# Performance work log

Hardware: AMD Instinct MI355X
Metric: run time of the kernel (lower is better)

## Reference

```python
import jax, jax.numpy as jnp
import numpy as np
from jax import lax

V, H, B, S, NSLOT, T, G, NSW = 20000, 400, 16, 256, 30, 10, 3, 40


def setup_inputs() -> dict:
    key = jax.random.key(0)
    ks = jax.random.split(key, 24)
    p = lambda k, shape: jax.random.normal(k, shape, dtype=jnp.float32) * 0.1
    return {
        'story': jax.random.randint(ks[0], (B, S), 0, V),
        'enc_lens': jax.random.randint(ks[1], (B,), S // 2, S + 1),
        'target_batches': jax.random.randint(ks[2], (B, NSLOT, T), 0, V),
        'domain_idx': jax.random.randint(ks[3], (NSLOT,), 0, NSW),
        'slot_idx': jax.random.randint(ks[4], (NSLOT,), 0, NSW),
        'emb': p(ks[5], (V, H)),
        'enc_Wih_f': p(ks[6], (3 * H, H)), 'enc_Whh_f': p(ks[7], (3 * H, H)),
        'enc_bih_f': p(ks[8], (3 * H,)), 'enc_bhh_f': p(ks[9], (3 * H,)),
        'enc_Wih_b': p(ks[10], (3 * H, H)), 'enc_Whh_b': p(ks[11], (3 * H, H)),
        'enc_bih_b': p(ks[12], (3 * H,)), 'enc_bhh_b': p(ks[13], (3 * H,)),
        'dec_Wih': p(ks[14], (3 * H, H)), 'dec_Whh': p(ks[15], (3 * H, H)),
        'dec_bih': p(ks[16], (3 * H,)), 'dec_bhh': p(ks[17], (3 * H,)),
        'Wr': p(ks[18], (1, 3 * H)), 'br': p(ks[19], (1,)),
        'Wg': p(ks[20], (G, H)), 'bg': p(ks[21], (G,)),
        'slot_table': p(ks[22], (NSW, H)),
    }


def _gru_scan(x, m, h0, Wih, Whh, bih, bhh):
    # x: [S,B,H], m: [S,B] validity mask (packed-sequence semantics)
    def step(h, xm):
        xt, mt = xm
        gi = xt @ Wih.T + bih
        gh = h @ Whh.T + bhh
        ir, iz, inn = jnp.split(gi, 3, -1)
        hr, hz, hn = jnp.split(gh, 3, -1)
        r = jax.nn.sigmoid(ir + hr)
        z = jax.nn.sigmoid(iz + hz)
        n = jnp.tanh(inn + r * hn)
        hnew = (1.0 - z) * n + z * h
        h = jnp.where(mt[:, None], hnew, h)
        y = jnp.where(mt[:, None], hnew, 0.0)
        return h, y
    hT, ys = lax.scan(step, h0, (x, m))
    return ys, hT


def reference(story, enc_lens, target_batches, domain_idx, slot_idx, emb,
              enc_Wih_f, enc_Whh_f, enc_bih_f, enc_bhh_f,
              enc_Wih_b, enc_Whh_b, enc_bih_b, enc_bhh_b,
              dec_Wih, dec_Whh, dec_bih, dec_bhh,
              Wr, br, Wg, bg, slot_table):
    Bc, Sc = story.shape
    nslot = domain_idx.shape[0]
    Tc = target_batches.shape[2]
    NB = nslot * Bc

    # ----- EncoderRNN: bidirectional GRU over story (seq-major) -----
    x = emb[story.T]                                   # [S,B,H]
    mask = jnp.arange(Sc)[:, None] < enc_lens[None, :]  # [S,B]
    h0 = jnp.zeros((Bc, H), jnp.float32)
    ys_f, h_f = _gru_scan(x, mask, h0, enc_Wih_f, enc_Whh_f, enc_bih_f, enc_bhh_f)
    ys_b, h_b = _gru_scan(x[::-1], mask[::-1], h0, enc_Wih_b, enc_Whh_b, enc_bih_b, enc_bhh_b)
    ys_b = ys_b[::-1]
    encoded_outputs = (ys_f + ys_b).transpose(1, 0, 2)  # [B,S,H]
    enc_hidden = h_f + h_b                              # [B,H]

    # ----- Generator (parallel decode, teacher forcing) -----
    combined = slot_table[domain_idx] + slot_table[slot_idx]           # [nslot,H]
    slot_emb_arr = jnp.repeat(combined[:, None, :], Bc, axis=1).reshape(NB, H)
    hidden0 = jnp.tile(enc_hidden, (nslot, 1))                         # [NB,H]
    enc_out = jnp.tile(encoded_outputs, (nslot, 1, 1))                 # [NB,S,H]
    lens_rep = jnp.tile(enc_lens, nslot)
    story_rep = jnp.tile(story, (nslot, 1))                            # [NB,S]
    attn_mask = jnp.arange(Sc)[None, :] < lens_rep[:, None]            # [NB,S]
    rows = jnp.arange(NB)[:, None]

    # teacher-forced decoder inputs: step0 = slot emb, then gold tokens
    tgt_flat = target_batches.transpose(1, 0, 2).reshape(NB, Tc)       # [NB,T]
    dec_in = jnp.concatenate([slot_emb_arr[None], emb[tgt_flat[:, :Tc - 1].T]], axis=0)  # [T,NB,H]

    def dec_step(h, x_in):
        gi = x_in @ dec_Wih.T + dec_bih
        gh = h @ dec_Whh.T + dec_bhh
        ir, iz, inn = jnp.split(gi, 3, -1)
        hr, hz, hn = jnp.split(gh, 3, -1)
        r = jax.nn.sigmoid(ir + hr)
        z = jax.nn.sigmoid(iz + hz)
        n = jnp.tanh(inn + r * hn)
        h = (1.0 - z) * n + z * h                      # dec_state == new hidden
        scores = jnp.einsum('nh,nsh->ns', h, enc_out)
        scores = jnp.where(attn_mask, scores, -jnp.inf)
        prob = jax.nn.softmax(scores, axis=1)          # [NB,S]
        context = jnp.einsum('ns,nsh->nh', prob, enc_out)
        p_vocab = jax.nn.softmax(h @ emb.T, axis=1)    # [NB,V]
        p_gen_vec = jnp.concatenate([h, context, x_in], axis=-1)
        sw = jax.nn.sigmoid(p_gen_vec @ Wr.T + br)     # [NB,1]
        p_ctx = jnp.zeros_like(p_vocab).at[rows, story_rep].add(prob)
        final_p = (1.0 - sw) * p_ctx + sw * p_vocab
        return h, (final_p, context)

    _, (finals, contexts) = lax.scan(dec_step, hidden0, dec_in)
    all_point_outputs = finals.reshape(Tc, nslot, Bc, V).transpose(1, 2, 0, 3)  # [nslot,B,T,V]
    all_gate_outputs = (contexts[0] @ Wg.T + bg).reshape(nslot, Bc, G)
    return all_point_outputs, all_gate_outputs
```

## Files before the change

kernel.cpp:

```cpp
#include <hip/hip_runtime.h>
#include <hip/hip_bf16.h>

typedef unsigned short u16;
typedef __attribute__((ext_vector_type(8))) short bf16x8;
typedef __attribute__((ext_vector_type(4))) float f32x4;
typedef __attribute__((ext_vector_type(4))) unsigned u32x4;

static constexpr int V = 20000, H = 400, B = 16, S = 256, NSLOT = 30, T = 10, G = 3;
static constexpr int H3 = 3 * H;
static constexpr int NB = NSLOT * B;
static constexpr int MM = T * NB;
static constexpr int ENBLK = 20;
static constexpr int ESL   = 20;
static constexpr int EROWS = 64;
static constexpr int EKP   = 416;
static constexpr int ENC_BLOCKS = 2 * ENBLK;
static constexpr int DGI_TM = (MM + 63) / 64;
static constexpr int DGI_TN = (H3 + 63) / 64;
static constexpr int DGI_TILES = DGI_TM * DGI_TN;
static constexpr int HP2 = 424;
static constexpr int SCP = 260;
static constexpr int PP  = 264;
static constexpr int CXP = 404;
static constexpr int FUSED_LDS = 32*HP2*2 + 32*SCP*4 + 32*PP*2 + 32*CXP*4;
static constexpr int NE = V * H;
static constexpr int NW = H3 * H;
static constexpr int NP = 2 * ENBLK * EROWS * EKP;

__device__ __forceinline__ float bf2f(u16 v) {
    union { unsigned u; float f; } x; x.u = ((unsigned)v) << 16; return x.f;
}
__device__ __forceinline__ u16 f2bf(float f) {
    union { float f; unsigned u; } x; x.f = f;
    unsigned r = x.u + 0x7fffu + ((x.u >> 16) & 1u);
    return (u16)(r >> 16);
}
__device__ __forceinline__ float sigm(float v) { return 1.f / (1.f + __expf(-v)); }

__global__ __launch_bounds__(256) void gemm_bt(
    const u16* __restrict__ A, const u16* __restrict__ Bt,
    const float* __restrict__ bias, float* __restrict__ C,
    int M, int N, int K, int lda, int ldb, long long ldc)
{
    __shared__ u16 As[64][40];
    __shared__ u16 Bs[64][40];
    const int m0 = blockIdx.x * 64, n0 = blockIdx.y * 64;
    const int tid = threadIdx.x, wave = tid >> 6, lane = tid & 63;
    const int wm = (wave >> 1) * 32, wn = (wave & 1) * 32;
    const int srow = tid >> 2, scol = (tid & 3) * 8;
    const int fr = lane & 15, kq = lane >> 4;
    f32x4 acc[2][2];
#pragma unroll
    for (int i = 0; i < 2; ++i)
#pragma unroll
        for (int j = 0; j < 2; ++j) acc[i][j] = (f32x4){0.f, 0.f, 0.f, 0.f};

    for (int k0 = 0; k0 < K; k0 += 32) {
        {
            int gr = m0 + srow, gc = k0 + scol;
            bf16x8 v;
            if (gr < M && gc + 8 <= K) {
                v = *(const bf16x8*)(A + (long long)gr * lda + gc);
            } else {
                short tmp[8];
#pragma unroll
                for (int j = 0; j < 8; ++j)
                    tmp[j] = (gr < M && gc + j < K) ? (short)A[(long long)gr * lda + gc + j] : (short)0;
                v = *(bf16x8*)tmp;
            }
            *(bf16x8*)&As[srow][scol] = v;
        }
        {
            int gr = n0 + srow, gc = k0 + scol;
            bf16x8 v;
            if (gr < N && gc + 8 <= K) {
                v = *(const bf16x8*)(Bt + (long long)gr * ldb + gc);
            } else {
                short tmp[8];
#pragma unroll
                for (int j = 0; j < 8; ++j)
                    tmp[j] = (gr < N && gc + j < K) ? (short)Bt[(long long)gr * ldb + gc + j] : (short)0;
                v = *(bf16x8*)tmp;
            }
            *(bf16x8*)&Bs[srow][scol] = v;
        }
        __syncthreads();
        bf16x8 af[2], bfr[2];
#pragma unroll
        for (int i = 0; i < 2; ++i) af[i]  = *(const bf16x8*)&As[wm + i * 16 + fr][kq * 8];
#pragma unroll
        for (int j = 0; j < 2; ++j) bfr[j] = *(const bf16x8*)&Bs[wn + j * 16 + fr][kq * 8];
#pragma unroll
        for (int i = 0; i < 2; ++i)
#pragma unroll
            for (int j = 0; j < 2; ++j)
                acc[i][j] = __builtin_amdgcn_mfma_f32_16x16x32_bf16(af[i], bfr[j], acc[i][j], 0, 0, 0);
        __syncthreads();
    }

#pragma unroll
    for (int i = 0; i < 2; ++i)
#pragma unroll
        for (int j = 0; j < 2; ++j) {
            int col = n0 + wn + j * 16 + fr;
            float bv = (bias != nullptr && col < N) ? bias[col] : 0.f;
#pragma unroll
            for (int r = 0; r < 4; ++r) {
                int row = m0 + wm + i * 16 + kq * 4 + r;
                if (row < M && col < N) C[(long long)row * ldc + col] = acc[i][j][r] + bv;
            }
        }
}

__global__ __launch_bounds__(256) void gemm_xw2_kernel(
    const u16* __restrict__ A,
    const u16* __restrict__ W0, const u16* __restrict__ W1,
    const float* __restrict__ b0, const float* __restrict__ b1,
    float* __restrict__ C0, float* __restrict__ C1)
{
    const int z = blockIdx.z;
    const u16* Bt = z ? W1 : W0;
    const float* bias = z ? b1 : b0;
    float* C = z ? C1 : C0;
    const int M = S * B, N = H3, K = H;

    __shared__ u16 As[64][40];
    __shared__ u16 Bs[64][40];
    const int m0 = blockIdx.x * 64, n0 = blockIdx.y * 64;
    const int tid = threadIdx.x, wave = tid >> 6, lane = tid & 63;
    const int wm = (wave >> 1) * 32, wn = (wave & 1) * 32;
    const int srow = tid >> 2, scol = (tid & 3) * 8;
    const int fr = lane & 15, kq = lane >> 4;
    f32x4 acc[2][2];
#pragma unroll
    for (int i = 0; i < 2; ++i)
#pragma unroll
        for (int j = 0; j < 2; ++j) acc[i][j] = (f32x4){0.f, 0.f, 0.f, 0.f};

    for (int k0 = 0; k0 < K; k0 += 32) {
        {
            int gr = m0 + srow, gc = k0 + scol;
            bf16x8 v = (bf16x8){0,0,0,0,0,0,0,0};
            if (gr < M && gc + 8 <= K) v = *(const bf16x8*)(A + (long long)gr * K + gc);
            *(bf16x8*)&As[srow][scol] = v;
        }
        {
            int gr = n0 + srow, gc = k0 + scol;
            bf16x8 v = (bf16x8){0,0,0,0,0,0,0,0};
            if (gr < N && gc + 8 <= K) v = *(const bf16x8*)(Bt + (long long)gr * K + gc);
            *(bf16x8*)&Bs[srow][scol] = v;
        }
        __syncthreads();
        bf16x8 af[2], bfr[2];
#pragma unroll
        for (int i = 0; i < 2; ++i) af[i]  = *(const bf16x8*)&As[wm + i * 16 + fr][kq * 8];
#pragma unroll
        for (int j = 0; j < 2; ++j) bfr[j] = *(const bf16x8*)&Bs[wn + j * 16 + fr][kq * 8];
#pragma unroll
        for (int i = 0; i < 2; ++i)
#pragma unroll
            for (int j = 0; j < 2; ++j)
                acc[i][j] = __builtin_amdgcn_mfma_f32_16x16x32_bf16(af[i], bfr[j], acc[i][j], 0, 0, 0);
        __syncthreads();
    }

#pragma unroll
    for (int i = 0; i < 2; ++i)
#pragma unroll
        for (int j = 0; j < 2; ++j) {
            int col = n0 + wn + j * 16 + fr;
            float bv = (col < N) ? bias[col] : 0.f;
#pragma unroll
            for (int r = 0; r < 4; ++r) {
                int row = m0 + wm + i * 16 + kq * 4 + r;
                if (row < M && col < N) C[(long long)row * H3 + col] = acc[i][j][r] + bv;
            }
        }
}

__global__ __launch_bounds__(256) void vocab_rowsum_kernel(
    const u16* __restrict__ A, const u16* __restrict__ Bt,
    float* __restrict__ rowsum)
{
    __shared__ u16 As[128][40];
    __shared__ u16 Bs[128][40];
    const int m0 = blockIdx.x * 128, n0 = blockIdx.y * 128;
    const int tid = threadIdx.x, wave = tid >> 6, lane = tid & 63;
    const int wm = (wave >> 1) * 64, wn = (wave & 1) * 64;
    const int srow = tid >> 1, scol = (tid & 1) * 16;
    const int fr = lane & 15, kq = lane >> 4;
    f32x4 acc[4][4];
#pragma unroll
    for (int i = 0; i < 4; ++i)
#pragma unroll
        for (int j = 0; j < 4; ++j) acc[i][j] = (f32x4){0.f, 0.f, 0.f, 0.f};

    for (int k0 = 0; k0 < H; k0 += 32) {
        {
            int gr = m0 + srow, gc = k0 + scol;
            bf16x8 v0 = (bf16x8){0,0,0,0,0,0,0,0}, v1 = v0;
            if (gr < MM) {
                const u16* src = A + (long long)gr * H + gc;
                if (gc + 8 <= H)  v0 = *(const bf16x8*)src;
                if (gc + 16 <= H) v1 = *(const bf16x8*)(src + 8);
            }
            *(bf16x8*)&As[srow][scol] = v0;
            *(bf16x8*)&As[srow][scol + 8] = v1;
        }
        {
            int gr = n0 + srow, gc = k0 + scol;
            bf16x8 v0 = (bf16x8){0,0,0,0,0,0,0,0}, v1 = v0;
            if (gr < V) {
                const u16* src = Bt + (long long)gr * H + gc;
                if (gc + 8 <= H)  v0 = *(const bf16x8*)src;
                if (gc + 16 <= H) v1 = *(const bf16x8*)(src + 8);
            }
            *(bf16x8*)&Bs[srow][scol] = v0;
            *(bf16x8*)&Bs[srow][scol + 8] = v1;
        }
        __syncthreads();
        bf16x8 af[4], bfr[4];
#pragma unroll
        for (int i = 0; i < 4; ++i) af[i]  = *(const bf16x8*)&As[wm + i * 16 + fr][kq * 8];
#pragma unroll
        for (int j = 0; j < 4; ++j) bfr[j] = *(const bf16x8*)&Bs[wn + j * 16 + fr][kq * 8];
#pragma unroll
        for (int i = 0; i < 4; ++i)
#pragma unroll
            for (int j = 0; j < 4; ++j)
                acc[i][j] = __builtin_amdgcn_mfma_f32_16x16x32_bf16(af[i], bfr[j], acc[i][j], 0, 0, 0);
        __syncthreads();
    }

#pragma unroll
    for (int i = 0; i < 4; ++i)
#pragma unroll
        for (int r = 0; r < 4; ++r) {
            int row = m0 + wm + i * 16 + kq * 4 + r;
            float s = 0.f;
#pragma unroll
            for (int j = 0; j < 4; ++j) {
                int col = n0 + wn + j * 16 + fr;
                if (row < MM && col < V) s += __expf(acc[i][j][r]);
            }
            s += __shfl_xor(s, 1); s += __shfl_xor(s, 2);
            s += __shfl_xor(s, 4); s += __shfl_xor(s, 8);
            if (fr == 0 && row < MM) atomicAdd(&rowsum[row], s);
        }
}

__global__ __launch_bounds__(256) void vocab_write_kernel(
    const u16* __restrict__ A, const u16* __restrict__ Bt,
    const float* __restrict__ swvT, const float* __restrict__ rowsum,
    float* __restrict__ C)
{
    __shared__ u16 As[128][40];
    __shared__ u16 Bs[128][40];
    const int m0 = blockIdx.x * 128, n0 = blockIdx.y * 128;
    const int tid = threadIdx.x, wave = tid >> 6, lane = tid & 63;
    const int wm = (wave >> 1) * 64, wn = (wave & 1) * 64;
    const int srow = tid >> 1, scol = (tid & 1) * 16;
    const int fr = lane & 15, kq = lane >> 4;
    f32x4 acc[4][4];
#pragma unroll
    for (int i = 0; i < 4; ++i)
#pragma unroll
        for (int j = 0; j < 4; ++j) acc[i][j] = (f32x4){0.f, 0.f, 0.f, 0.f};

    for (int k0 = 0; k0 < H; k0 += 32) {
        {
            int gr = m0 + srow, gc = k0 + scol;
            bf16x8 v0 = (bf16x8){0,0,0,0,0,0,0,0}, v1 = v0;
            if (gr < MM) {
                const u16* src = A + (long long)gr * H + gc;
                if (gc + 8 <= H)  v0 = *(const bf16x8*)src;
                if (gc + 16 <= H) v1 = *(const bf16x8*)(src + 8);
            }
            *(bf16x8*)&As[srow][scol] = v0;
            *(bf16x8*)&As[srow][scol + 8] = v1;
        }
        {
            int gr = n0 + srow, gc = k0 + scol;
            bf16x8 v0 = (bf16x8){0,0,0,0,0,0,0,0}, v1 = v0;
            if (gr < V) {
                const u16* src = Bt + (long long)gr * H + gc;
                if (gc + 8 <= H)  v0 = *(const bf16x8*)src;
                if (gc + 16 <= H) v1 = *(const bf16x8*)(src + 8);
            }
            *(bf16x8*)&Bs[srow][scol] = v0;
            *(bf16x8*)&Bs[srow][scol + 8] = v1;
        }
        __syncthreads();
        bf16x8 af[4], bfr[4];
#pragma unroll
        for (int i = 0; i < 4; ++i) af[i]  = *(const bf16x8*)&As[wm + i * 16 + fr][kq * 8];
#pragma unroll
        for (int j = 0; j < 4; ++j) bfr[j] = *(const bf16x8*)&Bs[wn + j * 16 + fr][kq * 8];
#pragma unroll
        for (int i = 0; i < 4; ++i)
#pragma unroll
            for (int j = 0; j < 4; ++j)
                acc[i][j] = __builtin_amdgcn_mfma_f32_16x16x32_bf16(af[i], bfr[j], acc[i][j], 0, 0, 0);
        __syncthreads();
    }

#pragma unroll
    for (int i = 0; i < 4; ++i)
#pragma unroll
        for (int r = 0; r < 4; ++r) {
            int row = m0 + wm + i * 16 + kq * 4 + r;
            float f = 0.f;
            if (row < MM) f = swvT[row] / rowsum[row];
#pragma unroll
            for (int j = 0; j < 4; ++j) {
                int col = n0 + wn + j * 16 + fr;
                if (row < MM && col < V) {
                    int n = row % NB, t = row / NB;
                    C[((long long)n * T + t) * V + col] = __expf(acc[i][j][r]) * f;
                }
            }
        }
}

__global__ void prep_all_kernel(
    const float* __restrict__ emb, u16* __restrict__ embb,
    const float* __restrict__ wihf, u16* __restrict__ wihfb,
    const float* __restrict__ wihb, u16* __restrict__ wihbb,
    const float* __restrict__ dwih, u16* __restrict__ dwihb,
    const float* __restrict__ dwhh, u16* __restrict__ dwhhb,
    const float* __restrict__ whhf, const float* __restrict__ whhb,
    u16* __restrict__ wencp)
{
    const int total = NE + 4 * NW + NP;
    for (int i = blockIdx.x * blockDim.x + threadIdx.x; i < total;
         i += gridDim.x * blockDim.x) {
        if (i < NE) { embb[i] = f2bf(emb[i]); continue; }
        int i2 = i - NE;
        if (i2 < NW) { wihfb[i2] = f2bf(wihf[i2]); continue; }
        i2 -= NW;
        if (i2 < NW) { wihbb[i2] = f2bf(wihb[i2]); continue; }
        i2 -= NW;
        if (i2 < NW) { dwihb[i2] = f2bf(dwih[i2]); continue; }
        i2 -= NW;
        if (i2 < NW) { dwhhb[i2] = f2bf(dwhh[i2]); continue; }
        i2 -= NW;
        int k = i2 % EKP; int r = i2 / EKP;
        int rloc = r % EROWS; r /= EROWS;
        int j = r % ENBLK; int dir = r / ENBLK;
        u16 v = 0;
        if (k < H && rloc < 3 * ESL) {
            int g = rloc / ESL, c = rloc % ESL;
            const float* W = dir ? whhb : whhf;
            v = f2bf(W[(long long)(g * H + j * ESL + c) * H + k]);
        }
        wencp[i2] = v;
    }
}

__global__ void embed_decin_kernel(
    const int* __restrict__ story, const u16* __restrict__ embb,
    u16* __restrict__ xb,
    const int* __restrict__ tgt, const int* __restrict__ dom,
    const int* __restrict__ sidx, const float* __restrict__ slt,
    u16* __restrict__ decin)
{
    int row = blockIdx.x;
    if (row < S * B) {
        int s = row >> 4, b = row & 15;
        int tok = story[b * S + s];
        const u16* e = embb + (long long)tok * H;
        u16* d = xb + (long long)row * H;
        for (int k = threadIdx.x; k < H; k += blockDim.x) d[k] = e[k];
    } else {
        int i = row - S * B;
        int t = i / NB, n = i % NB;
        int b = n & 15, slot = n >> 4;
        u16* d = decin + ((long long)t * NB + n) * H;
        if (t == 0) {
            const float* s1 = slt + (long long)dom[slot] * H;
            const float* s2 = slt + (long long)sidx[slot] * H;
            for (int k = threadIdx.x; k < H; k += blockDim.x) d[k] = f2bf(s1[k] + s2[k]);
        } else {
            int tok = tgt[(b * NSLOT + slot) * T + (t - 1)];
            const u16* e = embb + (long long)tok * H;
            for (int k = threadIdx.x; k < H; k += blockDim.x) d[k] = e[k];
        }
    }
}

__global__ __launch_bounds__(256) void enc_dgi_kernel(
    const u16* __restrict__ wencp,
    const float* __restrict__ bhhf, const float* __restrict__ bhhb,
    const float* __restrict__ gif, const float* __restrict__ gib,
    const int* __restrict__ lens,
    unsigned* __restrict__ hbuf, int* __restrict__ flags,
    float* __restrict__ ysf, float* __restrict__ ysb,
    float* __restrict__ hfo, float* __restrict__ hbo,
    const u16* __restrict__ decinb, const u16* __restrict__ dwhib,
    const float* __restrict__ dbih, float* __restrict__ dgi)
{
    __shared__ __align__(16) char ldsu[EROWS * EKP * 2 + EROWS * 17 * 4];
    const int tid = threadIdx.x, wave = tid >> 6, lane = tid & 63;
    const int fr = lane & 15, kq = lane >> 4;

    if (blockIdx.x >= ENC_BLOCKS) {
        u16* As = (u16*)ldsu;
        u16* Bs = As + 64 * 40;
        const int tile = blockIdx.x - ENC_BLOCKS;
        const int m0 = (tile % DGI_TM) * 64, n0 = (tile / DGI_TM) * 64;
        const int wm = (wave >> 1) * 32, wn = (wave & 1) * 32;
        const int srow = tid >> 2, scol = (tid & 3) * 8;
        f32x4 acc[2][2];
#pragma unroll
        for (int i = 0; i < 2; ++i)
#pragma unroll
            for (int j = 0; j < 2; ++j) acc[i][j] = (f32x4){0.f, 0.f, 0.f, 0.f};

        for (int k0 = 0; k0 < H; k0 += 32) {
            {
                int gr = m0 + srow, gc = k0 + scol;
                bf16x8 v = (bf16x8){0,0,0,0,0,0,0,0};
                if (gr < MM && gc + 8 <= H) v = *(const bf16x8*)(decinb + (long long)gr * H + gc);
                *(bf16x8*)&As[srow * 40 + scol] = v;
            }
            {
                int gr = n0 + srow, gc = k0 + scol;
                bf16x8 v = (bf16x8){0,0,0,0,0,0,0,0};
                if (gr < H3 && gc + 8 <= H) v = *(const bf16x8*)(dwhib + (long long)gr * H + gc);
                *(bf16x8*)&Bs[srow * 40 + scol] = v;
            }
            __syncthreads();
            bf16x8 af[2], bfr[2];
#pragma unroll
            for (int i = 0; i < 2; ++i) af[i]  = *(const bf16x8*)&As[(wm + i * 16 + fr) * 40 + kq * 8];
#pragma unroll
            for (int j = 0; j < 2; ++j) bfr[j] = *(const bf16x8*)&Bs[(wn + j * 16 + fr) * 40 + kq * 8];
#pragma unroll
            for (int i = 0; i < 2; ++i)
#pragma unroll
                for (int j = 0; j < 2; ++j)
                    acc[i][j] = __builtin_amdgcn_mfma_f32_16x16x32_bf16(af[i], bfr[j], acc[i][j], 0, 0, 0);
            __syncthreads();
        }
#pragma unroll
        for (int i = 0; i < 2; ++i)
#pragma unroll
            for (int j = 0; j < 2; ++j) {
                int col = n0 + wn + j * 16 + fr;
                float bv = (col < H3) ? dbih[col] : 0.f;
#pragma unroll
                for (int r = 0; r < 4; ++r) {
                    int row = m0 + wm + i * 16 + kq * 4 + r;
                    if (row < MM && col < H3) dgi[(long long)row * H3 + col] = acc[i][j][r] + bv;
                }
            }
        return;
    }

    u16* wlds = (u16*)ldsu;
    float* ghs = (float*)(ldsu + EROWS * EKP * 2);
    const int bid = blockIdx.x;
    const int dir = bid / ENBLK, j = bid % ENBLK;
    const float* bhh = dir ? bhhb : bhhf;
    const float* gi  = dir ? gib  : gif;
    float* ys = dir ? ysb : ysf;
    float* ho = dir ? hbo : hfo;

    const u16* wsrc = wencp + (long long)(dir * ENBLK + j) * EROWS * EKP;
    for (int i = tid * 8; i < EROWS * EKP; i += 256 * 8)
        *(bf16x8*)&wlds[i] = *(const bf16x8*)&wsrc[i];
    for (int i = tid; i < EROWS * 17; i += 256) ghs[i] = 0.f;

    const int p0 = tid, p1 = 256 + tid;
    const bool has1 = (tid < 64);
    const int b0 = p0 / ESL, kl0 = p0 % ESL;
    const int b1 = has1 ? p1 / ESL : 0, kl1 = has1 ? p1 % ESL : 0;
    const int k0 = j * ESL;
    const int len0 = lens[b0];
    const int len1 = has1 ? lens[b1] : 0;
    const float bhr0 = bhh[k0 + kl0], bhz0 = bhh[H + k0 + kl0], bhn0 = bhh[2 * H + k0 + kl0];
    const float bhr1 = has1 ? bhh[k0 + kl1] : 0.f;
    const float bhz1 = has1 ? bhh[H + k0 + kl1] : 0.f;
    const float bhn1 = has1 ? bhh[2 * H + k0 + kl1] : 0.f;
    float h0r = 0.f, h1r = 0.f;

    unsigned* hb_d = hbuf + (long long)dir * S * B * EKP;
    int* flg_d = flags + dir * S * ENBLK;
    const u16* arow = &wlds[(wave * 16 + fr) * EKP + kq * 8];
    __syncthreads();

    for (int t = 0; t < S; ++t) {
        const int s = dir ? (S - 1 - t) : t;
        const float* gbase = gi + (long long)s * B * H3;
        float gr0 = gbase[b0 * H3 + k0 + kl0];
        float gz0 = gbase[b0 * H3 + H + k0 + kl0];
        float gn0 = gbase[b0 * H3 + 2 * H + k0 + kl0];
        float gr1 = 0.f, gz1 = 0.f, gn1 = 0.f;
        if (has1) {
            gr1 = gbase[b1 * H3 + k0 + kl1];
            gz1 = gbase[b1 * H3 + H + k0 + kl1];
            gn1 = gbase[b1 * H3 + 2 * H + k0 + kl1];
        }

        f32x4 acc = (f32x4){0.f, 0.f, 0.f, 0.f};
        if (t > 0) {
            const int* fl = flg_d + (t - 1) * ENBLK;
            for (;;) {
                int v = 1;
                if (lane < ENBLK)
                    v = __hip_atomic_load(&fl[lane], __ATOMIC_RELAXED,
                                          __HIP_MEMORY_SCOPE_AGENT);
                if (__all(v != 0)) break;
                __builtin_amdgcn_s_sleep(2);
            }
            asm volatile("" ::: "memory");
            const unsigned* hrow = hb_d + ((long long)(t - 1) * B + fr) * EKP + kq * 8;
            f32x4 acch = (f32x4){0.f, 0.f, 0.f, 0.f};
            f32x4 accl = (f32x4){0.f, 0.f, 0.f, 0.f};
#pragma unroll
            for (int kk = 0; kk < 13; ++kk) {
                u32x4 a = *(const u32x4*)(hrow + kk * 32);
                u32x4 b = *(const u32x4*)(hrow + kk * 32 + 4);
                union { unsigned u[4]; bf16x8 v; } hi, lo;
                hi.u[0] = __builtin_amdgcn_perm(a[1], a[0], 0x05040100u);
                hi.u[1] = __builtin_amdgcn_perm(a[3], a[2], 0x05040100u);
                hi.u[2] = __builtin_amdgcn_perm(b[1], b[0], 0x05040100u);
                hi.u[3] = __builtin_amdgcn_perm(b[3], b[2], 0x05040100u);
                lo.u[0] = __builtin_amdgcn_perm(a[1], a[0], 0x07060302u);
                lo.u[1] = __builtin_amdgcn_perm(a[3], a[2], 0x07060302u);
                lo.u[2] = __builtin_amdgcn_perm(b[1], b[0], 0x07060302u);
                lo.u[3] = __builtin_amdgcn_perm(b[3], b[2], 0x07060302u);
                bf16x8 av = *(const bf16x8*)(arow + kk * 32);
                acch = __builtin_amdgcn_mfma_f32_16x16x32_bf16(av, hi.v, acch, 0, 0, 0);
                accl = __builtin_amdgcn_mfma_f32_16x16x32_bf16(av, lo.v, accl, 0, 0, 0);
            }
            acc = acch + accl;
        }
#pragma unroll
        for (int r = 0; r < 4; ++r) ghs[(wave * 16 + kq * 4 + r) * 17 + fr] = acc[r];
        __syncthreads();

        unsigned* hpub = hb_d + (long long)t * B * EKP;
        {
            float ghr = ghs[kl0 * 17 + b0];
            float ghz = ghs[(ESL + kl0) * 17 + b0];
            float ghn = ghs[(2 * ESL + kl0) * 17 + b0];
            float rg = sigm(gr0 + ghr + bhr0);
            float zg = sigm(gz0 + ghz + bhz0);
            float ng = tanhf(gn0 + rg * (ghn + bhn0));
            float hn = (1.f - zg) * ng + zg * h0r;
            bool msk = s < len0;
            float y = msk ? hn : 0.f;
            if (msk) h0r = hn;
            ys[((long long)(b0 * S + s)) * H + k0 + kl0] = y;
            u16 hi = f2bf(h0r);
            unsigned packed = (unsigned)hi | ((unsigned)f2bf(h0r - bf2f(hi)) << 16);
            __hip_atomic_store(&hpub[b0 * EKP + k0 + kl0], packed, __ATOMIC_RELAXED,
                               __HIP_MEMORY_SCOPE_AGENT);
        }
        if (has1) {
            float ghr = ghs[kl1 * 17 + b1];
            float ghz = ghs[(ESL + kl1) * 17 + b1];
            float ghn = ghs[(2 * ESL + kl1) * 17 + b1];
            float rg = sigm(gr1 + ghr + bhr1);
            float zg = sigm(gz1 + ghz + bhz1);
            float ng = tanhf(gn1 + rg * (ghn + bhn1));
            float hn = (1.f - zg) * ng + zg * h1r;
            bool msk = s < len1;
            float y = msk ? hn : 0.f;
            if (msk) h1r = hn;
            ys[((long long)(b1 * S + s)) * H + k0 + kl1] = y;
            u16 hi = f2bf(h1r);
            unsigned packed = (unsigned)hi | ((unsigned)f2bf(h1r - bf2f(hi)) << 16);
            __hip_atomic_store(&hpub[b1 * EKP + k0 + kl1], packed, __ATOMIC_RELAXED,
                               __HIP_MEMORY_SCOPE_AGENT);
        }
        __syncthreads();
        if (tid == 0)
            __hip_atomic_store(&flg_d[t * ENBLK + j], 1, __ATOMIC_RELAXED,
                               __HIP_MEMORY_SCOPE_AGENT);
    }
    ho[b0 * H + k0 + kl0] = h0r;
    if (has1) ho[b1 * H + k0 + kl1] = h1r;
}

__global__ __launch_bounds__(256) void packE_h0_kernel(
    const float* __restrict__ ysf, const float* __restrict__ ysb,
    u16* __restrict__ E, u16* __restrict__ ET,
    const float* __restrict__ hf, const float* __restrict__ hb,
    float* __restrict__ hf32, u16* __restrict__ hnk)
{
    __shared__ u16 tile[32][400];
    const int blk = blockIdx.x;
    if (blk < B * (S / 32)) {
        const int b = blk / (S / 32), s0 = (blk % (S / 32)) * 32;
        for (int si = 0; si < 32; ++si) {
            const long long base = ((long long)b * S + s0 + si) * H;
            for (int k = threadIdx.x; k < H; k += blockDim.x) {
                u16 v = f2bf(ysf[base + k] + ysb[base + k]);
                E[base + k] = v;
                tile[si][k] = v;
            }
        }
        __syncthreads();
        for (int idx = threadIdx.x; idx < 32 * H; idx += blockDim.x) {
            int k = idx >> 5, si = idx & 31;
            ET[((long long)b * H + k) * S + s0 + si] = tile[si][k];
        }
    } else {
        int n = blk - B * (S / 32), b = n & 15;
        for (int k = threadIdx.x; k < H; k += blockDim.x) {
            float v = hf[b * H + k] + hb[b * H + k];
            hf32[(long long)n * H + k] = v;
            hnk[(long long)n * H + k] = f2bf(v);
        }
    }
}

__global__ __launch_bounds__(512) void fused_step_kernel(
    const float* __restrict__ dgi, const float* __restrict__ dgh,
    float* __restrict__ hf32, u16* __restrict__ hall,
    const u16* __restrict__ decinb,
    const u16* __restrict__ Eb, const u16* __restrict__ ETb,
    const int* __restrict__ lens,
    const float* __restrict__ Wr, const float* __restrict__ br,
    const float* __restrict__ Wg, const float* __restrict__ bg,
    float* __restrict__ probfT, float* __restrict__ swvT,
    float* __restrict__ gout, int t)
{
    extern __shared__ char smem[];
    u16*   hls = (u16*)smem;
    float* scs = (float*)(smem + 32 * HP2 * 2);
    u16*   pls = (u16*)(smem + 32 * HP2 * 2 + 32 * SCP * 4);
    float* cxs = (float*)(smem + 32 * HP2 * 2 + 32 * SCP * 4 + 32 * PP * 2);

    const int b = blockIdx.x;
    const int tid = threadIdx.x, wave = tid >> 6, lane = tid & 63;
    const int fr = lane & 15, kq = lane >> 4;
    const int len = lens[b];

    for (int i = tid; i < 32 * (HP2 - H); i += 512) {
        int r = i / (HP2 - H), c = H + i % (HP2 - H);
        hls[r * HP2 + c] = 0;
    }
    for (int i = tid; i < 2 * HP2; i += 512) hls[30 * HP2 + i] = 0;
    for (int i = tid; i < 2 * PP; i += 512) pls[30 * PP + i] = 0;

    for (int i = tid; i < 30 * H; i += 512) {
        int slot = i / H, k = i % H;
        int n = slot * 16 + b;
        const float* gi = dgi + ((long long)t * NB + n) * H3;
        const float* gh = dgh + (long long)n * H3;
        float r  = sigm(gi[k] + gh[k]);
        float z  = sigm(gi[H + k] + gh[H + k]);
        float nn = tanhf(gi[2 * H + k] + r * gh[2 * H + k]);
        float h  = hf32[(long long)n * H + k];
        float hn = (1.f - z) * nn + z * h;
        hf32[(long long)n * H + k] = hn;
        u16 hb = f2bf(hn);
        hall[((long long)t * NB + n) * H + k] = hb;
        hls[slot * HP2 + k] = hb;
    }
    __syncthreads();

    {
        const int nt0 = wave * 2;
        f32x4 acc[2][2];
#pragma unroll
        for (int i = 0; i < 2; ++i)
#pragma unroll
            for (int jj = 0; jj < 2; ++jj) acc[i][jj] = (f32x4){0.f, 0.f, 0.f, 0.f};
        const u16* br0 = Eb + ((long long)b * S + nt0 * 16 + fr) * H + kq * 8;
        const u16* br1 = Eb + ((long long)b * S + (nt0 + 1) * 16 + fr) * H + kq * 8;
        const u16* ar0 = hls + fr * HP2 + kq * 8;
        const u16* ar1 = hls + (16 + fr) * HP2 + kq * 8;
#pragma unroll
        for (int kk = 0; kk < 13; ++kk) {
            bf16x8 av0 = *(const bf16x8*)(ar0 + kk * 32);
            bf16x8 av1 = *(const bf16x8*)(ar1 + kk * 32);
            bf16x8 bv0, bv1;
            if (kk == 12 && kq >= 2) {
                bv0 = (bf16x8){0,0,0,0,0,0,0,0}; bv1 = bv0;
            } else {
                bv0 = *(const bf16x8*)(br0 + kk * 32);
                bv1 = *(const bf16x8*)(br1 + kk * 32);
            }
            acc[0][0] = __builtin_amdgcn_mfma_f32_16x16x32_bf16(av0, bv0, acc[0][0], 0, 0, 0);
            acc[1][0] = __builtin_amdgcn_mfma_f32_16x16x32_bf16(av1, bv0, acc[1][0], 0, 0, 0);
            acc[0][1] = __builtin_amdgcn_mfma_f32_16x16x32_bf16(av0, bv1, acc[0][1], 0, 0, 0);
            acc[1][1] = __builtin_amdgcn_mfma_f32_16x16x32_bf16(av1, bv1, acc[1][1], 0, 0, 0);
        }
#pragma unroll
        for (int i = 0; i < 2; ++i)
#pragma unroll
            for (int jj = 0; jj < 2; ++jj)
#pragma unroll
                for (int r = 0; r < 4; ++r)
                    scs[(i * 16 + kq * 4 + r) * SCP + (nt0 + jj) * 16 + fr] = acc[i][jj][r];
    }
    __syncthreads();

    for (int i = 0; i < 4; ++i) {
        int row = wave * 4 + i;
        if (row >= 30) break;
        int n = row * 16 + b;
        float v[4];
        float mx = -3.0e38f;
#pragma unroll
        for (int q = 0; q < 4; ++q) {
            int s = lane + 64 * q;
            float x = (s < len) ? scs[row * SCP + s] : -3.0e38f;
            v[q] = x; mx = fmaxf(mx, x);
        }
        mx = fmaxf(mx, __shfl_xor(mx, 1));  mx = fmaxf(mx, __shfl_xor(mx, 2));
        mx = fmaxf(mx, __shfl_xor(mx, 4));  mx = fmaxf(mx, __shfl_xor(mx, 8));
        mx = fmaxf(mx, __shfl_xor(mx, 16)); mx = fmaxf(mx, __shfl_xor(mx, 32));
        float sum = 0.f;
#pragma unroll
        for (int q = 0; q < 4; ++q) {
            int s = lane + 64 * q;
            float e = (s < len) ? __expf(v[q] - mx) : 0.f;
            v[q] = e; sum += e;
        }
        sum += __shfl_xor(sum, 1);  sum += __shfl_xor(sum, 2);
        sum += __shfl_xor(sum, 4);  sum += __shfl_xor(sum, 8);
        sum += __shfl_xor(sum, 16); sum += __shfl_xor(sum, 32);
        float inv = 1.f / sum;
#pragma unroll
        for (int q = 0; q < 4; ++q) {
            int s = lane + 64 * q;
            float pr = v[q] * inv;
            pls[row * PP + s] = f2bf(pr);
            probfT[((long long)(t * NB + n)) * S + s] = pr;
        }
    }
    __syncthreads();

    for (int nt = wave; nt < 25; nt += 8) {
        f32x4 acc0 = (f32x4){0.f,0.f,0.f,0.f}, acc1 = (f32x4){0.f,0.f,0.f,0.f};
        const u16* brow = ETb + ((long long)b * H + nt * 16 + fr) * S + kq * 8;
        const u16* ar0 = pls + fr * PP + kq * 8;
        const u16* ar1 = pls + (16 + fr) * PP + kq * 8;
#pragma unroll
        for (int kk = 0; kk < 8; ++kk) {
            bf16x8 bv  = *(const bf16x8*)(brow + kk * 32);
            bf16x8 av0 = *(const bf16x8*)(ar0 + kk * 32);
            bf16x8 av1 = *(const bf16x8*)(ar1 + kk * 32);
            acc0 = __builtin_amdgcn_mfma_f32_16x16x32_bf16(av0, bv, acc0, 0, 0, 0);
            acc1 = __builtin_amdgcn_mfma_f32_16x16x32_bf16(av1, bv, acc1, 0, 0, 0);
        }
#pragma unroll
        for (int r = 0; r < 4; ++r) {
            cxs[(kq * 4 + r) * CXP + nt * 16 + fr] = acc0[r];
            cxs[(16 + kq * 4 + r) * CXP + nt * 16 + fr] = acc1[r];
        }
    }
    __syncthreads();

    for (int i = 0; i < 4; ++i) {
        int slot = wave + 8 * i;
        if (slot >= 30) break;
        int n = slot * 16 + b;
        const u16* xrow = decinb + ((long long)t * NB + n) * H;
        float p = 0.f;
        for (int k = lane; k < H; k += 64)
            p += bf2f(hls[slot * HP2 + k]) * Wr[k]
               + cxs[slot * CXP + k] * Wr[H + k]
               + bf2f(xrow[k]) * Wr[2 * H + k];
        p += __shfl_xor(p, 1);  p += __shfl_xor(p, 2);
        p += __shfl_xor(p, 4);  p += __shfl_xor(p, 8);
        p += __shfl_xor(p, 16); p += __shfl_xor(p, 32);
        if (lane == 0) swvT[t * NB + n] = sigm(p + br[0]);
        if (t == 0) {
            for (int g = 0; g < G; ++g) {
                float q = 0.f;
                for (int k = lane; k < H; k += 64)
                    q += cxs[slot * CXP + k] * Wg[g * H + k];
                q += __shfl_xor(q, 1);  q += __shfl_xor(q, 2);
                q += __shfl_xor(q, 4);  q += __shfl_xor(q, 8);
                q += __shfl_xor(q, 16); q += __shfl_xor(q, 32);
                if (lane == 0) gout[(long long)n * G + g] = q + bg[g];
            }
        }
    }
}

__global__ void scatter_all_kernel(float* __restrict__ out, const int* __restrict__ story,
                                   const int* __restrict__ lens, const float* __restrict__ swvT,
                                   const float* __restrict__ probfT) {
    const int n = blockIdx.x, t = blockIdx.y, b = n & 15, s = threadIdx.x;
    if (s < lens[b]) {
        int tok = story[b * S + s];
        atomicAdd(out + ((long long)n * T + t) * V + tok,
                  (1.f - swvT[t * NB + n]) * probfT[((long long)(t * NB + n)) * S + s]);
    }
}

extern "C" void kernel_launch(void* const* d_in, const int* in_sizes, int n_in,
                              void* d_out, int out_size, void* d_ws, size_t ws_size,
                              hipStream_t stream) {
    const int*   story = (const int*)d_in[0];
    const int*   lens  = (const int*)d_in[1];
    const int*   tgt   = (const int*)d_in[2];
    const int*   dom   = (const int*)d_in[3];
    const int*   sidx  = (const int*)d_in[4];
    const float* emb   = (const float*)d_in[5];
    const float* wihf  = (const float*)d_in[6];
    const float* whhf  = (const float*)d_in[7];
    const float* bihf  = (const float*)d_in[8];
    const float* bhhf  = (const float*)d_in[9];
    const float* wihb  = (const float*)d_in[10];
    const float* whhb  = (const float*)d_in[11];
    const float* bihb  = (const float*)d_in[12];
    const float* bhhb  = (const float*)d_in[13];
    const float* dwih  = (const float*)d_in[14];
    const float* dwhh  = (const float*)d_in[15];
    const float* dbih  = (const float*)d_in[16];
    const float* dbhh  = (const float*)d_in[17];
    const float* Wr    = (const float*)d_in[18];
    const float* br    = (const float*)d_in[19];
    const float* Wg    = (const float*)d_in[20];
    const float* bg    = (const float*)d_in[21];
    const float* slt   = (const float*)d_in[22];
    float* out = (float*)d_out;

    char* wsb = (char*)d_ws;
    size_t off = 0;
    auto alloc = [&](size_t bytes) -> char* {
        char* p = wsb + off;
        off += (bytes + 255) & ~(size_t)255;
        return p;
    };
    u16*   embb   = (u16*)alloc((size_t)V * H * 2);
    u16*   wihfb  = (u16*)alloc((size_t)H3 * H * 2);
    u16*   wihbb  = (u16*)alloc((size_t)H3 * H * 2);
    u16*   dwihb  = (u16*)alloc((size_t)H3 * H * 2);
    u16*   dwhhb  = (u16*)alloc((size_t)H3 * H * 2);
    u16*   wencp  = (u16*)alloc((size_t)2 * ENBLK * EROWS * EKP * 2);
    unsigned* hbuf = (unsigned*)alloc((size_t)2 * S * B * EKP * 4);
    int*   flags  = (int*)alloc((size_t)2 * S * ENBLK * 4);
    u16*   xb     = (u16*)alloc((size_t)S * B * H * 2);
    u16*   decinb = (u16*)alloc((size_t)T * NB * H * 2);
    float* gif    = (float*)alloc((size_t)S * B * H3 * 4);
    float* gib    = (float*)alloc((size_t)S * B * H3 * 4);
    float* dgi    = (float*)alloc((size_t)T * NB * H3 * 4);
    float* ysf    = (float*)alloc((size_t)B * S * H * 4);
    float* ysb    = (float*)alloc((size_t)B * S * H * 4);
    float* hfv    = (float*)alloc((size_t)B * H * 4);
    float* hbv    = (float*)alloc((size_t)B * H * 4);
    u16*   Eb     = (u16*)alloc((size_t)B * S * H * 2);
    u16*   ETb    = (u16*)alloc((size_t)B * H * S * 2);
    float* hf32   = (float*)alloc((size_t)NB * H * 4);
    u16*   hnk    = (u16*)alloc((size_t)NB * H * 2);
    u16*   hall   = (u16*)alloc((size_t)T * NB * H * 2);
    float* dgh    = (float*)alloc((size_t)NB * H3 * 4);
    float* probfT = (float*)alloc((size_t)T * NB * S * 4);
    float* swvT   = (float*)alloc((size_t)T * NB * 4);
    float* rowsumT = (float*)alloc((size_t)T * NB * 4);
    (void)ws_size; (void)in_sizes; (void)n_in; (void)out_size;

    hipFuncSetAttribute((const void*)fused_step_kernel,
                        hipFuncAttributeMaxDynamicSharedMemorySize, FUSED_LDS);

    hipMemsetAsync(flags, 0, (size_t)2 * S * ENBLK * 4, stream);
    hipMemsetAsync(hbuf, 0, (size_t)2 * S * B * EKP * 4, stream);
    hipMemsetAsync(rowsumT, 0, (size_t)T * NB * 4, stream);
    prep_all_kernel<<<2048, 256, 0, stream>>>(emb, embb, wihf, wihfb, wihb, wihbb,
                                              dwih, dwihb, dwhh, dwhhb,
                                              whhf, whhb, wencp);
    embed_decin_kernel<<<S * B + T * NB, 256, 0, stream>>>(
        story, embb, xb, tgt, dom, sidx, slt, decinb);
    {
        dim3 g((S * B + 63) / 64, (H3 + 63) / 64, 2);
        gemm_xw2_kernel<<<g, 256, 0, stream>>>(xb, wihfb, wihbb, bihf, bihb, gif, gib);
    }

    enc_dgi_kernel<<<ENC_BLOCKS + DGI_TILES, 256, 0, stream>>>(
        wencp, bhhf, bhhb, gif, gib, lens, hbuf, flags, ysf, ysb, hfv, hbv,
        decinb, dwihb, dbih, dgi);
    packE_h0_kernel<<<B * (S / 32) + NB, 256, 0, stream>>>(
        ysf, ysb, Eb, ETb, hfv, hbv, hf32, hnk);

    for (int t = 0; t < T; ++t) {
        const u16* hprev = (t == 0) ? hnk : hall + (size_t)(t - 1) * NB * H;
        {
            dim3 g((NB + 63) / 64, (H3 + 63) / 64);
            gemm_bt<<<g, 256, 0, stream>>>(hprev, dwhhb, dbhh, dgh,
                                           NB, H3, H, H, H, H3);
        }
        fused_step_kernel<<<16, 512, FUSED_LDS, stream>>>(
            dgi, dgh, hf32, hall, decinb, Eb, ETb, lens, Wr, br, Wg, bg,
            probfT, swvT, out + (size_t)NB * T * V, t);
    }

    {
        dim3 g((MM + 127) / 128, (V + 127) / 128);
        vocab_rowsum_kernel<<<g, 256, 0, stream>>>(hall, embb, rowsumT);
        vocab_write_kernel<<<g, 256, 0, stream>>>(hall, embb, swvT, rowsumT, out);
    }
    { dim3 g(NB, T); scatter_all_kernel<<<g, 256, 0, stream>>>(out, story, lens, swvT, probfT); }
}
```

Before: 2.306 ms.

## Split GRU cell into wide kernel and co-schedule next-step Whh GEMM with attention

The per-step GRU elementwise update moves out of the 16-block attention kernel into its own 750-block grid-stride kernel, so it is spread across many CUs. The next step's hidden-to-hidden GEMM is merged into the attention kernel as extra blocks that run alongside the 16 attention blocks, and the first GEMM is hoisted before the loop. The GEMM tile loader also drops its scalar edge-case fallback in favour of zero-fill. Launches per step stay at two, but the GEMM blocks now use 512-thread blocks with only 4 active waves and the large dynamic LDS reservation, which may limit occupancy.

After: 2.075 ms (median of 2 runs). 1.11x faster.

```diff
diff --git a/kernel.cpp b/kernel.cpp
--- a/kernel.cpp
+++ b/kernel.cpp
@@ -18,6 +18,9 @@
 static constexpr int DGI_TM = (MM + 63) / 64;
 static constexpr int DGI_TN = (H3 + 63) / 64;
 static constexpr int DGI_TILES = DGI_TM * DGI_TN;
+static constexpr int DGH_TM = (NB + 63) / 64;
+static constexpr int DGH_TN = (H3 + 63) / 64;
+static constexpr int DGH_TILES = DGH_TM * DGH_TN;
 static constexpr int HP2 = 424;
 static constexpr int SCP = 260;
 static constexpr int PP  = 264;
@@ -58,30 +61,14 @@
     for (int k0 = 0; k0 < K; k0 += 32) {
         {
             int gr = m0 + srow, gc = k0 + scol;
-            bf16x8 v;
-            if (gr < M && gc + 8 <= K) {
-                v = *(const bf16x8*)(A + (long long)gr * lda + gc);
-            } else {
-                short tmp[8];
-#pragma unroll
-                for (int j = 0; j < 8; ++j)
-                    tmp[j] = (gr < M && gc + j < K) ? (short)A[(long long)gr * lda + gc + j] : (short)0;
-                v = *(bf16x8*)tmp;
-            }
+            bf16x8 v = (bf16x8){0,0,0,0,0,0,0,0};
+            if (gr < M && gc + 8 <= K) v = *(const bf16x8*)(A + (long long)gr * lda + gc);
             *(bf16x8*)&As[srow][scol] = v;
         }
         {
             int gr = n0 + srow, gc = k0 + scol;
-            bf16x8 v;
-            if (gr < N && gc + 8 <= K) {
-                v = *(const bf16x8*)(Bt + (long long)gr * ldb + gc);
-            } else {
-                short tmp[8];
-#pragma unroll
-                for (int j = 0; j < 8; ++j)
-                    tmp[j] = (gr < N && gc + j < K) ? (short)Bt[(long long)gr * ldb + gc + j] : (short)0;
-                v = *(bf16x8*)tmp;
-            }
+            bf16x8 v = (bf16x8){0,0,0,0,0,0,0,0};
+            if (gr < N && gc + 8 <= K) v = *(const bf16x8*)(Bt + (long long)gr * ldb + gc);
             *(bf16x8*)&Bs[srow][scol] = v;
         }
         __syncthreads();
@@ -617,9 +604,28 @@
     }
 }
 
-__global__ __launch_bounds__(512) void fused_step_kernel(
+__global__ __launch_bounds__(256) void gru_cell_kernel(
     const float* __restrict__ dgi, const float* __restrict__ dgh,
-    float* __restrict__ hf32, u16* __restrict__ hall,
+    float* __restrict__ hf32, u16* __restrict__ hall, int t)
+{
+    const int total = NB * H;
+    for (int i = blockIdx.x * 256 + threadIdx.x; i < total; i += gridDim.x * 256) {
+        int n = i / H, k = i % H;
+        const float* gi = dgi + ((long long)t * NB + n) * H3;
+        const float* gh = dgh + (long long)n * H3;
+        float r  = sigm(gi[k] + gh[k]);
+        float z  = sigm(gi[H + k] + gh[H + k]);
+        float nn = tanhf(gi[2 * H + k] + r * gh[2 * H + k]);
+        float h  = hf32[i];
+        float hn = (1.f - z) * nn + z * h;
+        hf32[i] = hn;
+        hall[((long long)t * NB + n) * H + k] = f2bf(hn);
+    }
+}
+
+__global__ __launch_bounds__(512) void dec_attn_kernel(
+    const u16* __restrict__ hall, const u16* __restrict__ dwhhb,
+    const float* __restrict__ dbhh, float* __restrict__ dgh,
     const u16* __restrict__ decinb,
     const u16* __restrict__ Eb, const u16* __restrict__ ETb,
     const int* __restrict__ lens,
@@ -629,14 +635,79 @@
     float* __restrict__ gout, int t)
 {
     extern __shared__ char smem[];
+    const int tid = threadIdx.x, wave = tid >> 6, lane = tid & 63;
+    const int fr = lane & 15, kq = lane >> 4;
+    const u16* hcur = hall + (long long)t * NB * H;
+
+    if (blockIdx.x < DGH_TILES) {
+        if (t == T - 1) return;
+        u16* As = (u16*)smem;
+        u16* Bs = As + 64 * 40;
+        const int tile = blockIdx.x;
+        const int m0 = (tile % DGH_TM) * 64, n0 = (tile / DGH_TM) * 64;
+        const bool act = (wave < 4);
+        const int wm = (wave >> 1) * 32, wn = (wave & 1) * 32;
+        const int srow = tid >> 2, scol = (tid & 3) * 8;
+        f32x4 acc[2][2];
+#pragma unroll
+        for (int i = 0; i < 2; ++i)
+#pragma unroll
+            for (int j = 0; j < 2; ++j) acc[i][j] = (f32x4){0.f, 0.f, 0.f, 0.f};
+
+        for (int k0 = 0; k0 < H; k0 += 32) {
+            if (tid < 256) {
+                {
+                    int gr = m0 + srow, gc = k0 + scol;
+                    bf16x8 v = (bf16x8){0,0,0,0,0,0,0,0};
+                    if (gr < NB && gc + 8 <= H) v = *(const bf16x8*)(hcur + (long long)gr * H + gc);
+                    *(bf16x8*)&As[srow * 40 + scol] = v;
+                }
+                {
+                    int gr = n0 + srow, gc = k0 + scol;
+                    bf16x8 v = (bf16x8){0,0,0,0,0,0,0,0};
+                    if (gr < H3 && gc + 8 <= H) v = *(const bf16x8*)(dwhhb + (long long)gr * H + gc);
+                    *(bf16x8*)&Bs[srow * 40 + scol] = v;
+                }
+            }
+            __syncthreads();
+            if (act) {
+                bf16x8 af[2], bfr[2];
+#pragma unroll
+                for (int i = 0; i < 2; ++i) af[i]  = *(const bf16x8*)&As[(wm + i * 16 + fr) * 40 + kq * 8];
+#pragma unroll
+                for (int j = 0; j < 2; ++j) bfr[j] = *(const bf16x8*)&Bs[(wn + j * 16 + fr) * 40 + kq * 8];
+#pragma unroll
+                for (int i = 0; i < 2; ++i)
+#pragma unroll
+                    for (int j = 0; j < 2; ++j)
+                        acc[i][j] = __builtin_amdgcn_mfma_f32_16x16x32_bf16(af[i], bfr[j], acc[i][j], 0, 0, 0);
+            }
+            __syncthreads();
+        }
+        if (act) {
+#pragma unroll
+            for (int i = 0; i < 2; ++i)
+#pragma unroll
+                for (int j = 0; j < 2; ++j) {
+                    int col = n0 + wn + j * 16 + fr;
+                    float bv = (col < H3) ? dbhh[col] : 0.f;
+#pragma unroll
+                    for (int r = 0; r < 4; ++r) {
+                        int row = m0 + wm + i * 16 + kq * 4 + r;
+                        if (row < NB && col < H3)
+                            dgh[(long long)row * H3 + col] = acc[i][j][r] + bv;
+                    }
+                }
+        }
+        return;
+    }
+
     u16*   hls = (u16*)smem;
     float* scs = (float*)(smem + 32 * HP2 * 2);
     u16*   pls = (u16*)(smem + 32 * HP2 * 2 + 32 * SCP * 4);
     float* cxs = (float*)(smem + 32 * HP2 * 2 + 32 * SCP * 4 + 32 * PP * 2);
 
-    const int b = blockIdx.x;
-    const int tid = threadIdx.x, wave = tid >> 6, lane = tid & 63;
-    const int fr = lane & 15, kq = lane >> 4;
+    const int b = blockIdx.x - DGH_TILES;
     const int len = lens[b];
 
     for (int i = tid; i < 32 * (HP2 - H); i += 512) {
@@ -648,18 +719,7 @@
 
     for (int i = tid; i < 30 * H; i += 512) {
         int slot = i / H, k = i % H;
-        int n = slot * 16 + b;
-        const float* gi = dgi + ((long long)t * NB + n) * H3;
-        const float* gh = dgh + (long long)n * H3;
-        float r  = sigm(gi[k] + gh[k]);
-        float z  = sigm(gi[H + k] + gh[H + k]);
-        float nn = tanhf(gi[2 * H + k] + r * gh[2 * H + k]);
-        float h  = hf32[(long long)n * H + k];
-        float hn = (1.f - z) * nn + z * h;
-        hf32[(long long)n * H + k] = hn;
-        u16 hb = f2bf(hn);
-        hall[((long long)t * NB + n) * H + k] = hb;
-        hls[slot * HP2 + k] = hb;
+        hls[slot * HP2 + k] = hcur[((long long)(slot * 16 + b)) * H + k];
     }
     __syncthreads();
 
@@ -859,7 +919,7 @@
     float* rowsumT = (float*)alloc((size_t)T * NB * 4);
     (void)ws_size; (void)in_sizes; (void)n_in; (void)out_size;
 
-    hipFuncSetAttribute((const void*)fused_step_kernel,
+    hipFuncSetAttribute((const void*)dec_attn_kernel,
                         hipFuncAttributeMaxDynamicSharedMemorySize, FUSED_LDS);
 
     hipMemsetAsync(flags, 0, (size_t)2 * S * ENBLK * 4, stream);
@@ -881,16 +941,15 @@
     packE_h0_kernel<<<B * (S / 32) + NB, 256, 0, stream>>>(
         ysf, ysb, Eb, ETb, hfv, hbv, hf32, hnk);
 
+    {
+        dim3 g((NB + 63) / 64, (H3 + 63) / 64);
+        gemm_bt<<<g, 256, 0, stream>>>(hnk, dwhhb, dbhh, dgh, NB, H3, H, H, H, H3);
+    }
     for (int t = 0; t < T; ++t) {
-        const u16* hprev = (t == 0) ? hnk : hall + (size_t)(t - 1) * NB * H;
-        {
-            dim3 g((NB + 63) / 64, (H3 + 63) / 64);
-            gemm_bt<<<g, 256, 0, stream>>>(hprev, dwhhb, dbhh, dgh,
-                                           NB, H3, H, H, H, H3);
-        }
-        fused_step_kernel<<<16, 512, FUSED_LDS, stream>>>(
-            dgi, dgh, hf32, hall, decinb, Eb, ETb, lens, Wr, br, Wg, bg,
-            probfT, swvT, out + (size_t)NB * T * V, t);
+        gru_cell_kernel<<<750, 256, 0, stream>>>(dgi, dgh, hf32, hall, t);
+        dec_attn_kernel<<<DGH_TILES + 16, 512, FUSED_LDS, stream>>>(
+            hall, dwhhb, dbhh, dgh, decinb, Eb, ETb, lens,
+            Wr, br, Wg, bg, probfT, swvT, out + (size_t)NB * T * V, t);
     }
 
     {
```
